# Optimization experiments

Measured on AMD Instinct MI355X. Metric: run time of the kernel, lower is better.

Reference implementation:

```python
import jax, jax.numpy as jnp
import numpy as np

E = 200000          # number of edges
MUL = 32            # multiplicity per irrep in irreps_in1/irreps_out
NT = 2              # num_tensors_in1
U = MUL * NT        # 64: combined multiplicity after fuse_in
SCALAR_DIM = 64     # irreps_edge_scalars num_irreps
HID = 64            # radial MLP hidden width
WNUM = 2 * U        # 128: LinearScaleWithWeights weight_numel (64 for 0e + 64 for 1o)
PW = 0.125          # uvw path weight sqrt(dim_out/ (u*v)) combined with 3j: all paths -> 1/8
INV_S3 = 1.0 / np.sqrt(3.0)

# e3nn normalize2mom constant for silu: 1/sqrt(E[silu(z)^2]), z ~ N(0,1)
_z = np.linspace(-12.0, 12.0, 200001)
_phi = np.exp(-0.5 * _z ** 2) / np.sqrt(2.0 * np.pi)
_s = _z / (1.0 + np.exp(-_z))
SILU_CST = float(1.0 / np.sqrt(np.trapz(_s ** 2 * _phi, _z)))


def setup_inputs() -> dict:
    key = jax.random.key(0)
    ks = jax.random.split(key, 15)
    f32 = jnp.float32
    return {
        "x1a": jax.random.normal(ks[0], (E, 128), f32),   # 32x0e + 32x1o
        "x1b": jax.random.normal(ks[1], (E, 128), f32),
        "x2": jax.random.normal(ks[2], (E, 4), f32),      # 1x0e + 1x1o
        "scalars": jax.random.normal(ks[3], (E, SCALAR_DIM), f32),
        # main tensor-product weights, one (u=64, w=32) block per instruction (v=1 squeezed)
        "w0": jax.random.normal(ks[4], (U, MUL), f32),    # 0e x 0e -> 0e (slot 0)
        "w1": jax.random.normal(ks[5], (U, MUL), f32),    # 1o x 1o -> 0e (slot 1)
        "w2": jax.random.normal(ks[6], (U, MUL), f32),    # 0e x 1o -> 1o (slot 2)
        "w3": jax.random.normal(ks[7], (U, MUL), f32),    # 1o x 0e -> 1o (slot 3)
        # LinearScaleWithWeights.linear_out: 64x0e+64x1o -> 32x0e+32x1o
        "Wl0": jax.random.normal(ks[8], (U, MUL), f32),
        "Wl1": jax.random.normal(ks[9], (U, MUL), f32),
        # radial MLP (e3nn FullyConnectedNet [64,64,64,128], silu)
        "Wm1": jax.random.normal(ks[10], (SCALAR_DIM, HID), f32),
        "Wm2": jax.random.normal(ks[11], (HID, HID), f32),
        "Wm3": jax.random.normal(ks[12], (HID, WNUM), f32),
        # final o3.Linear: 32x0e+32x1o -> 32x0e+32x1o
        "Wf0": jax.random.normal(ks[13], (MUL, MUL), f32),
        "Wf1": jax.random.normal(ks[14], (MUL, MUL), f32),
    }


def reference(x1a, x1b, x2, scalars, w0, w1, w2, w3, Wl0, Wl1, Wm1, Wm2, Wm3, Wf0, Wf1):
    n = x1a.shape[0]
    # fuse_in: stack heads then regroup per irrep -> combined 64x0e + 64x1o layout
    s0 = jnp.concatenate([x1a[:, :MUL], x1b[:, :MUL]], axis=1)                    # [E, 64]
    s1 = jnp.concatenate([x1a[:, MUL:].reshape(n, MUL, 3),
                          x1b[:, MUL:].reshape(n, MUL, 3)], axis=1)               # [E, 64, 3]
    y0 = x2[:, 0:1]    # 1x0e
    y1 = x2[:, 1:4]    # 1x1o

    # weight generator: e3nn FullyConnectedNet with normalized silu
    h = SILU_CST * jax.nn.silu((scalars @ Wm1) / jnp.sqrt(jnp.float32(SCALAR_DIM)))
    h = SILU_CST * jax.nn.silu((h @ Wm2) / jnp.sqrt(jnp.float32(HID)))
    weights = (h @ Wm3) / jnp.sqrt(jnp.float32(HID))                              # [E, 128]

    # main TensorProduct -> irreps_mid = 32x0e + 32x0e + 32x1o + 32x1o
    mid0 = PW * jnp.einsum('eu,uw->ew', s0 * y0, w0)                              # [E, 32]
    mid1 = (PW * INV_S3) * jnp.einsum('eu,uw->ew',
                                      jnp.einsum('euk,ek->eu', s1, y1), w1)       # [E, 32]
    mid2 = PW * jnp.einsum('eu,uw,ek->ewk', s0, w2, y1)                           # [E, 32, 3]
    mid3 = PW * jnp.einsum('euk,uw->ewk', s1 * y0[:, :, None], w3)                # [E, 32, 3]
    m0 = jnp.concatenate([mid0, mid1], axis=1)                                    # [E, 64] 0e
    m1 = jnp.concatenate([mid2, mid3], axis=1)                                    # [E, 64, 3] 1o

    # LinearScaleWithWeights: per-edge elementwise scale (uvu tp vs ones), then o3.Linear
    m0 = m0 * weights[:, :U]
    m1 = m1 * weights[:, U:, None]
    o0 = jnp.einsum('eu,uw->ew', m0, Wl0) / jnp.sqrt(jnp.float32(U))              # [E, 32]
    o1 = jnp.einsum('euk,uw->ewk', m1, Wl1) / jnp.sqrt(jnp.float32(U))            # [E, 32, 3]

    # final o3.Linear on irreps_out
    o0 = jnp.einsum('eu,uw->ew', o0, Wf0) / jnp.sqrt(jnp.float32(MUL))
    o1 = jnp.einsum('euk,uw->ewk', o1, Wf1) / jnp.sqrt(jnp.float32(MUL))
    return jnp.concatenate([o0, o1.reshape(n, MUL * 3)], axis=1)                  # [E, 128]
```

## Files before the change

### kernel.cpp

```cpp
#include <hip/hip_runtime.h>
#include <math.h>


#define TPB 256
#define ET  64
#define SAS 68

#define FMA4(acc, s, b)                                         \
  acc.x = fmaf((s), (b).x, acc.x); acc.y = fmaf((s), (b).y, acc.y); \
  acc.z = fmaf((s), (b).z, acc.z); acc.w = fmaf((s), (b).w, acc.w)

__global__ void zero_cst_kernel(double* cst) {
  if (threadIdx.x == 0) cst[0] = 0.0;
}

__global__ void cst_accum_kernel(double* cst) {
  __shared__ double red[256];
  double sum = 0.0;
  for (long i = (long)blockIdx.x * 256 + threadIdx.x; i <= 200000; i += 64L * 256) {
    double z = -12.0 + (double)i * (24.0 / 200000.0);
    double s = z / (1.0 + exp(-z));
    double phi = exp(-0.5 * z * z) * 0.3989422804014327;
    double f = s * s * phi;
    if (i == 0 || i == 200000) f *= 0.5;
    sum += f;
  }
  red[threadIdx.x] = sum;
  __syncthreads();
  for (int off = 128; off > 0; off >>= 1) {
    if (threadIdx.x < (unsigned)off) red[threadIdx.x] += red[threadIdx.x + off];
    __syncthreads();
  }
  if (threadIdx.x == 0) atomicAdd(cst, red[0]);
}

__global__ void prep_C_kernel(const float* __restrict__ Wl0, const float* __restrict__ Wf0,
                              const float* __restrict__ Wl1, const float* __restrict__ Wf1,
                              float* __restrict__ C0, float* __restrict__ C1) {
  const float* Wl = blockIdx.x ? Wl1 : Wl0;
  const float* Wf = blockIdx.x ? Wf1 : Wf0;
  float* C = blockIdx.x ? C1 : C0;
  for (int i = threadIdx.x; i < 64 * 32; i += 256) {
    int u = i >> 5, w = i & 31;
    float acc = 0.f;
#pragma unroll
    for (int v = 0; v < 32; ++v) acc = fmaf(Wl[u * 32 + v], Wf[v * 32 + w], acc);
    C[i] = acc * 0.022097086912079612f;
  }
}

__device__ __forceinline__ void stageB(const float* __restrict__ g, int ncols, int col0,
                                       float* __restrict__ sB, int t) {
#pragma unroll
  for (int r = 0; r < 2; ++r) {
    int i = (r * TPB + t) * 4;
    int c = i >> 5, j = i & 31;
    *(float4*)(sB + i) = *(const float4*)(g + c * ncols + col0 + j);
  }
}

__device__ __forceinline__ void gemm2(const float* __restrict__ sA,
                                      const float* __restrict__ sB,
                                      int e0l, int e1l, int cg,
                                      float4& out0, float4& out1) {
  float4 acc0 = make_float4(0.f, 0.f, 0.f, 0.f);
  float4 acc1 = make_float4(0.f, 0.f, 0.f, 0.f);
  const float* a0p = sA + e0l * SAS;
  const float* a1p = sA + e1l * SAS;
  const float* bp  = sB + 4 * cg;
#pragma unroll 4
  for (int c4 = 0; c4 < 16; ++c4) {
    float4 a0 = *(const float4*)(a0p + 4 * c4);
    float4 a1 = *(const float4*)(a1p + 4 * c4);
    const float* bb = bp + c4 * 128;
    float4 b0 = *(const float4*)(bb);
    float4 b1 = *(const float4*)(bb + 32);
    float4 b2 = *(const float4*)(bb + 64);
    float4 b3 = *(const float4*)(bb + 96);
    FMA4(acc0, a0.x, b0); FMA4(acc1, a1.x, b0);
    FMA4(acc0, a0.y, b1); FMA4(acc1, a1.y, b1);
    FMA4(acc0, a0.z, b2); FMA4(acc1, a1.z, b2);
    FMA4(acc0, a0.w, b3); FMA4(acc1, a1.w, b3);
  }
  out0 = acc0;
  out1 = acc1;
}

__device__ __forceinline__ float silu1(float x, float cst) {
  x *= 0.125f;
  return cst * x / (1.f + __expf(-x));
}

__device__ __forceinline__ float4 siluq(float4 v, float cst) {
  return make_float4(silu1(v.x, cst), silu1(v.y, cst), silu1(v.z, cst), silu1(v.w, cst));
}

__device__ __forceinline__ float4 muls(float4 a, float s) {
  return make_float4(a.x * s, a.y * s, a.z * s, a.w * s);
}

__device__ __forceinline__ float4 cmul(float4 a, float4 b, float s) {
  return make_float4(s * a.x * b.x, s * a.y * b.y, s * a.z * b.z, s * a.w * b.w);
}

__global__ __launch_bounds__(TPB, 4) void fused_tp(
    const float* __restrict__ x1a, const float* __restrict__ x1b,
    const float* __restrict__ x2, const float* __restrict__ scalars,
    const float* __restrict__ w0, const float* __restrict__ w1,
    const float* __restrict__ w2, const float* __restrict__ w3,
    const float* __restrict__ Wm1, const float* __restrict__ Wm2,
    const float* __restrict__ Wm3, const float* __restrict__ C0,
    const float* __restrict__ C1, const double* __restrict__ cstp,
    float* __restrict__ out) {
  __shared__ float sA[ET * SAS];
  __shared__ float sB0[64 * 32];
  __shared__ float sB1[64 * 32];
  __shared__ float sY[ET * 4];

  const int t  = threadIdx.x;
  const int cg = t & 7;
  const int eh = t >> 3;
  const long e0 = (long)blockIdx.x * ET;
  const float cst = (float)(1.0 / sqrt(cstp[0] * (24.0 / 200000.0)));

  const float pw   = 0.125f;
  const float pws3 = 0.125f * 0.57735026918962576f;

  if (t < ET) *(float4*)(sY + 4 * t) = *(const float4*)(x2 + (e0 + t) * 4);
#pragma unroll
  for (int r = 0; r < 4; ++r) {
    int i = r * TPB + t; int e = i >> 4; int j4 = (i & 15) << 2;
    *(float4*)(sA + e * SAS + j4) = *(const float4*)(scalars + (e0 + e) * 64 + j4);
  }
  stageB(Wm1, 64, 0, sB0, t);
  stageB(Wm1, 64, 32, sB1, t);
  __syncthreads();

  float4 h0a, h0b, h1a, h1b;
  {
    float4 r0, r1;
    gemm2(sA, sB0, eh, eh + 32, cg, r0, r1);
    h0a = siluq(r0, cst); h1a = siluq(r1, cst);
    gemm2(sA, sB1, eh, eh + 32, cg, r0, r1);
    h0b = siluq(r0, cst); h1b = siluq(r1, cst);
  }
  __syncthreads();

  *(float4*)(sA + eh * SAS + 4 * cg)        = h0a;
  *(float4*)(sA + eh * SAS + 32 + 4 * cg)   = h0b;
  *(float4*)(sA + (eh + 32) * SAS + 4 * cg)      = h1a;
  *(float4*)(sA + (eh + 32) * SAS + 32 + 4 * cg) = h1b;
  stageB(Wm2, 64, 0, sB0, t);
  stageB(Wm2, 64, 32, sB1, t);
  __syncthreads();

  {
    float4 r0, r1;
    gemm2(sA, sB0, eh, eh + 32, cg, r0, r1);
    h0a = siluq(r0, cst); h1a = siluq(r1, cst);
    gemm2(sA, sB1, eh, eh + 32, cg, r0, r1);
    h0b = siluq(r0, cst); h1b = siluq(r1, cst);
  }
  __syncthreads();

  *(float4*)(sA + eh * SAS + 4 * cg)        = h0a;
  *(float4*)(sA + eh * SAS + 32 + 4 * cg)   = h0b;
  *(float4*)(sA + (eh + 32) * SAS + 4 * cg)      = h1a;
  *(float4*)(sA + (eh + 32) * SAS + 32 + 4 * cg) = h1b;
  stageB(Wm3, 128, 0, sB0, t);
  stageB(Wm3, 128, 32, sB1, t);
  __syncthreads();

  float4 wq[2][4];
  {
    float4 r0, r1;
    gemm2(sA, sB0, eh, eh + 32, cg, r0, r1);
    wq[0][0] = muls(r0, 0.125f); wq[1][0] = muls(r1, 0.125f);
    gemm2(sA, sB1, eh, eh + 32, cg, r0, r1);
    wq[0][1] = muls(r0, 0.125f); wq[1][1] = muls(r1, 0.125f);
  }
  __syncthreads();
  stageB(Wm3, 128, 64, sB0, t);
  stageB(Wm3, 128, 96, sB1, t);
  __syncthreads();
  {
    float4 r0, r1;
    gemm2(sA, sB0, eh, eh + 32, cg, r0, r1);
    wq[0][2] = muls(r0, 0.125f); wq[1][2] = muls(r1, 0.125f);
    gemm2(sA, sB1, eh, eh + 32, cg, r0, r1);
    wq[0][3] = muls(r0, 0.125f); wq[1][3] = muls(r1, 0.125f);
  }
  __syncthreads();

#pragma unroll
  for (int r = 0; r < 4; ++r) {
    int i = r * TPB + t; int e = i >> 4; int j4 = (i & 15) << 2;
    const float* src = (j4 < 32) ? (x1a + (e0 + e) * 128 + j4)
                                 : (x1b + (e0 + e) * 128 + j4 - 32);
    *(float4*)(sA + e * SAS + j4) = *(const float4*)src;
  }
  stageB(w0, 32, 0, sB0, t);
  stageB(w2, 32, 0, sB1, t);
  __syncthreads();
  float4 m0q[2], p2q[2];
  gemm2(sA, sB0, eh, eh + 32, cg, m0q[0], m0q[1]);
  gemm2(sA, sB1, eh, eh + 32, cg, p2q[0], p2q[1]);
  __syncthreads();

#pragma unroll 2
  for (int r = 0; r < 16; ++r) {
    int i = r * TPB + t; int e = i >> 6; int u = i & 63;
    const float* xr = ((u < 32) ? x1a : x1b) + (e0 + e) * 128 + 32 + 3 * (u & 31);
    const float* yr = sY + e * 4;
    sA[e * SAS + u] = xr[0] * yr[1] + xr[1] * yr[2] + xr[2] * yr[3];
  }
  stageB(w1, 32, 0, sB0, t);
  stageB(w3, 32, 0, sB1, t);
  __syncthreads();
  float4 m1q[2];
  gemm2(sA, sB0, eh, eh + 32, cg, m1q[0], m1q[1]);
  __syncthreads();

#pragma unroll
  for (int ei = 0; ei < 2; ++ei) {
    int e = eh + 32 * ei;
    float y0v = sY[e * 4];
    *(float4*)(sA + e * SAS + 4 * cg)      = cmul(m0q[ei], wq[ei][0], pw * y0v);
    *(float4*)(sA + e * SAS + 32 + 4 * cg) = cmul(m1q[ei], wq[ei][1], pws3);
  }
  stageB(C0, 32, 0, sB0, t);
  __syncthreads();
  float4 o0q[2];
  gemm2(sA, sB0, eh, eh + 32, cg, o0q[0], o0q[1]);
  __syncthreads();

  stageB(C1, 32, 0, sB0, t);
  float o1v[2][12];
#pragma unroll
  for (int k = 0; k < 3; ++k) {
#pragma unroll 2
    for (int r = 0; r < 16; ++r) {
      int i = r * TPB + t; int e = i >> 6; int u = i & 63;
      const float* xr = ((u < 32) ? x1a : x1b) + (e0 + e) * 128 + 32 + 3 * (u & 31);
      sA[e * SAS + u] = xr[k];
    }
    __syncthreads();
    float4 t3[2];
    gemm2(sA, sB1, eh, eh + 32, cg, t3[0], t3[1]);
    __syncthreads();
#pragma unroll
    for (int ei = 0; ei < 2; ++ei) {
      int e = eh + 32 * ei;
      float y0v = sY[e * 4];
      float y1k = sY[e * 4 + 1 + k];
      *(float4*)(sA + e * SAS + 4 * cg)      = cmul(p2q[ei], wq[ei][2], pw * y1k);
      *(float4*)(sA + e * SAS + 32 + 4 * cg) = cmul(t3[ei], wq[ei][3], pw * y0v);
    }
    __syncthreads();
    float4 r0, r1;
    gemm2(sA, sB0, eh, eh + 32, cg, r0, r1);
    o1v[0][0 + k] = r0.x; o1v[0][3 + k] = r0.y; o1v[0][6 + k] = r0.z; o1v[0][9 + k] = r0.w;
    o1v[1][0 + k] = r1.x; o1v[1][3 + k] = r1.y; o1v[1][6 + k] = r1.z; o1v[1][9 + k] = r1.w;
    __syncthreads();
  }

#pragma unroll
  for (int ei = 0; ei < 2; ++ei) {
    long eg = e0 + eh + 32 * ei;
    float* ob = out + eg * 128;
    *(float4*)(ob + 4 * cg) = o0q[ei];
    float* o1b = ob + 32 + 12 * cg;
    *(float4*)(o1b)     = make_float4(o1v[ei][0], o1v[ei][1], o1v[ei][2],  o1v[ei][3]);
    *(float4*)(o1b + 4) = make_float4(o1v[ei][4], o1v[ei][5], o1v[ei][6],  o1v[ei][7]);
    *(float4*)(o1b + 8) = make_float4(o1v[ei][8], o1v[ei][9], o1v[ei][10], o1v[ei][11]);
  }
}

extern "C" void kernel_launch(void* const* d_in, const int* in_sizes, int n_in,
                              void* d_out, int out_size, void* d_ws, size_t ws_size,
                              hipStream_t stream) {
  const float* x1a     = (const float*)d_in[0];
  const float* x1b     = (const float*)d_in[1];
  const float* x2      = (const float*)d_in[2];
  const float* scalars = (const float*)d_in[3];
  const float* w0      = (const float*)d_in[4];
  const float* w1      = (const float*)d_in[5];
  const float* w2      = (const float*)d_in[6];
  const float* w3      = (const float*)d_in[7];
  const float* Wl0     = (const float*)d_in[8];
  const float* Wl1     = (const float*)d_in[9];
  const float* Wm1     = (const float*)d_in[10];
  const float* Wm2     = (const float*)d_in[11];
  const float* Wm3     = (const float*)d_in[12];
  const float* Wf0     = (const float*)d_in[13];
  const float* Wf1     = (const float*)d_in[14];
  float* out = (float*)d_out;

  double* cst = (double*)d_ws;
  float* C0 = (float*)d_ws + 128;
  float* C1 = C0 + 64 * 32;

  const int E = in_sizes[0] / 128;
  const int nblocks = E / ET;

  zero_cst_kernel<<<1, 64, 0, stream>>>(cst);
  cst_accum_kernel<<<64, 256, 0, stream>>>(cst);
  prep_C_kernel<<<2, 256, 0, stream>>>(Wl0, Wf0, Wl1, Wf1, C0, C1);
  fused_tp<<<nblocks, TPB, 0, stream>>>(x1a, x1b, x2, scalars, w0, w1, w2, w3,
                                        Wm1, Wm2, Wm3, C0, C1, cst, out);
}
```

Measured before the change: 481.4 us.

## Hoist k-independent GEMMs out of the 1o loop and merge prep kernels

```diff
diff --git a/kernel.cpp b/kernel.cpp
--- a/kernel.cpp
+++ b/kernel.cpp
@@ -3,49 +3,46 @@
 
 
 #define TPB 256
-#define ET  64
 #define SAS 68
 
 #define FMA4(acc, s, b)                                         \
   acc.x = fmaf((s), (b).x, acc.x); acc.y = fmaf((s), (b).y, acc.y); \
   acc.z = fmaf((s), (b).z, acc.z); acc.w = fmaf((s), (b).w, acc.w)
 
-__global__ void zero_cst_kernel(double* cst) {
-  if (threadIdx.x == 0) cst[0] = 0.0;
-}
-
-__global__ void cst_accum_kernel(double* cst) {
-  __shared__ double red[256];
-  double sum = 0.0;
-  for (long i = (long)blockIdx.x * 256 + threadIdx.x; i <= 200000; i += 64L * 256) {
-    double z = -12.0 + (double)i * (24.0 / 200000.0);
-    double s = z / (1.0 + exp(-z));
-    double phi = exp(-0.5 * z * z) * 0.3989422804014327;
-    double f = s * s * phi;
-    if (i == 0 || i == 200000) f *= 0.5;
-    sum += f;
-  }
-  red[threadIdx.x] = sum;
-  __syncthreads();
-  for (int off = 128; off > 0; off >>= 1) {
-    if (threadIdx.x < (unsigned)off) red[threadIdx.x] += red[threadIdx.x + off];
-    __syncthreads();
-  }
-  if (threadIdx.x == 0) atomicAdd(cst, red[0]);
-}
-
-__global__ void prep_C_kernel(const float* __restrict__ Wl0, const float* __restrict__ Wf0,
-                              const float* __restrict__ Wl1, const float* __restrict__ Wf1,
-                              float* __restrict__ C0, float* __restrict__ C1) {
-  const float* Wl = blockIdx.x ? Wl1 : Wl0;
-  const float* Wf = blockIdx.x ? Wf1 : Wf0;
-  float* C = blockIdx.x ? C1 : C0;
-  for (int i = threadIdx.x; i < 64 * 32; i += 256) {
-    int u = i >> 5, w = i & 31;
-    float acc = 0.f;
-#pragma unroll
-    for (int v = 0; v < 32; ++v) acc = fmaf(Wl[u * 32 + v], Wf[v * 32 + w], acc);
-    C[i] = acc * 0.022097086912079612f;
+__global__ void prep_kernel(const float* __restrict__ Wl0, const float* __restrict__ Wf0,
+                            const float* __restrict__ Wl1, const float* __restrict__ Wf1,
+                            float* __restrict__ C0, float* __restrict__ C1,
+                            double* __restrict__ part) {
+  if (blockIdx.x < 64) {
+    __shared__ double red[256];
+    double sum = 0.0;
+    for (long i = (long)blockIdx.x * 256 + threadIdx.x; i <= 200000; i += 64L * 256) {
+      double z = -12.0 + (double)i * (24.0 / 200000.0);
+      double s = z / (1.0 + exp(-z));
+      double phi = exp(-0.5 * z * z) * 0.3989422804014327;
+      double f = s * s * phi;
+      if (i == 0 || i == 200000) f *= 0.5;
+      sum += f;
+    }
+    red[threadIdx.x] = sum;
+    __syncthreads();
+    for (int off = 128; off > 0; off >>= 1) {
+      if (threadIdx.x < (unsigned)off) red[threadIdx.x] += red[threadIdx.x + off];
+      __syncthreads();
+    }
+    if (threadIdx.x == 0) part[blockIdx.x] = red[0];
+  } else {
+    const int b = blockIdx.x - 64;
+    const float* Wl = b ? Wl1 : Wl0;
+    const float* Wf = b ? Wf1 : Wf0;
+    float* C = b ? C1 : C0;
+    for (int i = threadIdx.x; i < 64 * 32; i += 256) {
+      int u = i >> 5, w = i & 31;
+      float acc = 0.f;
+#pragma unroll
+      for (int v = 0; v < 32; ++v) acc = fmaf(Wl[u * 32 + v], Wf[v * 32 + w], acc);
+      C[i] = acc * 0.022097086912079612f;
+    }
   }
 }
 
@@ -86,6 +83,73 @@
   out1 = acc1;
 }
 
+__device__ __forceinline__ void gemm2_dual(const float* __restrict__ sA,
+                                           const float* __restrict__ sB0,
+                                           const float* __restrict__ sB1,
+                                           int e0l, int e1l, int cg,
+                                           float4& o00, float4& o01,
+                                           float4& o10, float4& o11) {
+  float4 a00 = make_float4(0.f, 0.f, 0.f, 0.f);
+  float4 a01 = make_float4(0.f, 0.f, 0.f, 0.f);
+  float4 a10 = make_float4(0.f, 0.f, 0.f, 0.f);
+  float4 a11 = make_float4(0.f, 0.f, 0.f, 0.f);
+  const float* a0p = sA + e0l * SAS;
+  const float* a1p = sA + e1l * SAS;
+  const float* bp0 = sB0 + 4 * cg;
+  const float* bp1 = sB1 + 4 * cg;
+#pragma unroll 2
+  for (int c4 = 0; c4 < 16; ++c4) {
+    float4 a0 = *(const float4*)(a0p + 4 * c4);
+    float4 a1 = *(const float4*)(a1p + 4 * c4);
+    const float* b0b = bp0 + c4 * 128;
+    const float* b1b = bp1 + c4 * 128;
+    float4 B00 = *(const float4*)(b0b);
+    float4 B01 = *(const float4*)(b0b + 32);
+    float4 B02 = *(const float4*)(b0b + 64);
+    float4 B03 = *(const float4*)(b0b + 96);
+    float4 B10 = *(const float4*)(b1b);
+    float4 B11 = *(const float4*)(b1b + 32);
+    float4 B12 = *(const float4*)(b1b + 64);
+    float4 B13 = *(const float4*)(b1b + 96);
+    FMA4(a00, a0.x, B00); FMA4(a01, a1.x, B00);
+    FMA4(a10, a0.x, B10); FMA4(a11, a1.x, B10);
+    FMA4(a00, a0.y, B01); FMA4(a01, a1.y, B01);
+    FMA4(a10, a0.y, B11); FMA4(a11, a1.y, B11);
+    FMA4(a00, a0.z, B02); FMA4(a01, a1.z, B02);
+    FMA4(a10, a0.z, B12); FMA4(a11, a1.z, B12);
+    FMA4(a00, a0.w, B03); FMA4(a01, a1.w, B03);
+    FMA4(a10, a0.w, B13); FMA4(a11, a1.w, B13);
+  }
+  o00 = a00; o01 = a01; o10 = a10; o11 = a11;
+}
+
+__device__ __forceinline__ void gemm_k32(const float* __restrict__ sA,
+                                         const float* __restrict__ sBbase,
+                                         int e0l, int e1l, int cg,
+                                         float4& out0, float4& out1) {
+  float4 acc0 = make_float4(0.f, 0.f, 0.f, 0.f);
+  float4 acc1 = make_float4(0.f, 0.f, 0.f, 0.f);
+  const float* a0p = sA + e0l * SAS;
+  const float* a1p = sA + e1l * SAS;
+  const float* bp  = sBbase + 4 * cg;
+#pragma unroll 4
+  for (int c4 = 0; c4 < 8; ++c4) {
+    float4 a0 = *(const float4*)(a0p + 4 * c4);
+    float4 a1 = *(const float4*)(a1p + 4 * c4);
+    const float* bb = bp + c4 * 128;
+    float4 b0 = *(const float4*)(bb);
+    float4 b1 = *(const float4*)(bb + 32);
+    float4 b2 = *(const float4*)(bb + 64);
+    float4 b3 = *(const float4*)(bb + 96);
+    FMA4(acc0, a0.x, b0); FMA4(acc1, a1.x, b0);
+    FMA4(acc0, a0.y, b1); FMA4(acc1, a1.y, b1);
+    FMA4(acc0, a0.z, b2); FMA4(acc1, a1.z, b2);
+    FMA4(acc0, a0.w, b3); FMA4(acc1, a1.w, b3);
+  }
+  out0 = acc0;
+  out1 = acc1;
+}
+
 __device__ __forceinline__ float silu1(float x, float cst) {
   x *= 0.125f;
   return cst * x / (1.f + __expf(-x));
@@ -101,6 +165,10 @@
 
 __device__ __forceinline__ float4 cmul(float4 a, float4 b, float s) {
   return make_float4(s * a.x * b.x, s * a.y * b.y, s * a.z * b.z, s * a.w * b.w);
+}
+
+__device__ __forceinline__ float4 emul(float4 a, float4 b) {
+  return make_float4(a.x * b.x, a.y * b.y, a.z * b.z, a.w * b.w);
 }
 
 __global__ __launch_bounds__(TPB, 4) void fused_tp(
@@ -110,23 +178,29 @@
     const float* __restrict__ w2, const float* __restrict__ w3,
     const float* __restrict__ Wm1, const float* __restrict__ Wm2,
     const float* __restrict__ Wm3, const float* __restrict__ C0,
-    const float* __restrict__ C1, const double* __restrict__ cstp,
+    const float* __restrict__ C1, const double* __restrict__ part,
     float* __restrict__ out) {
-  __shared__ float sA[ET * SAS];
-  __shared__ float sB0[64 * 32];
-  __shared__ float sB1[64 * 32];
-  __shared__ float sY[ET * 4];
+  __shared__ __align__(16) float sA[64 * SAS];
+  __shared__ __align__(16) float sB0[64 * 32];
+  __shared__ __align__(16) float sB1[64 * 32];
+  __shared__ __align__(16) float sY[64 * 4];
+  __shared__ float scst_s;
 
   const int t  = threadIdx.x;
   const int cg = t & 7;
   const int eh = t >> 3;
-  const long e0 = (long)blockIdx.x * ET;
-  const float cst = (float)(1.0 / sqrt(cstp[0] * (24.0 / 200000.0)));
+  const long e0 = (long)blockIdx.x * 64;
 
   const float pw   = 0.125f;
   const float pws3 = 0.125f * 0.57735026918962576f;
 
-  if (t < ET) *(float4*)(sY + 4 * t) = *(const float4*)(x2 + (e0 + t) * 4);
+  if (t < 64) {
+    double v = part[t];
+#pragma unroll
+    for (int m = 32; m > 0; m >>= 1) v += __shfl_xor(v, m);
+    if (t == 0) scst_s = (float)(1.0 / sqrt(v * (24.0 / 200000.0)));
+    *(float4*)(sY + 4 * t) = *(const float4*)(x2 + (e0 + t) * 4);
+  }
 #pragma unroll
   for (int r = 0; r < 4; ++r) {
     int i = r * TPB + t; int e = i >> 4; int j4 = (i & 15) << 2;
@@ -136,60 +210,42 @@
   stageB(Wm1, 64, 32, sB1, t);
   __syncthreads();
 
-  float4 h0a, h0b, h1a, h1b;
-  {
-    float4 r0, r1;
-    gemm2(sA, sB0, eh, eh + 32, cg, r0, r1);
-    h0a = siluq(r0, cst); h1a = siluq(r1, cst);
-    gemm2(sA, sB1, eh, eh + 32, cg, r0, r1);
-    h0b = siluq(r0, cst); h1b = siluq(r1, cst);
-  }
-  __syncthreads();
-
-  *(float4*)(sA + eh * SAS + 4 * cg)        = h0a;
-  *(float4*)(sA + eh * SAS + 32 + 4 * cg)   = h0b;
-  *(float4*)(sA + (eh + 32) * SAS + 4 * cg)      = h1a;
-  *(float4*)(sA + (eh + 32) * SAS + 32 + 4 * cg) = h1b;
+  const float cst = scst_s;
+  const float4 yv0 = *(const float4*)(sY + eh * 4);
+  const float4 yv1 = *(const float4*)(sY + (eh + 32) * 4);
+
+  float4 r00, r01, r10, r11;
+  gemm2_dual(sA, sB0, sB1, eh, eh + 32, cg, r00, r01, r10, r11);
+  __syncthreads();
+  *(float4*)(sA + eh * SAS + 4 * cg)             = siluq(r00, cst);
+  *(float4*)(sA + eh * SAS + 32 + 4 * cg)        = siluq(r10, cst);
+  *(float4*)(sA + (eh + 32) * SAS + 4 * cg)      = siluq(r01, cst);
+  *(float4*)(sA + (eh + 32) * SAS + 32 + 4 * cg) = siluq(r11, cst);
   stageB(Wm2, 64, 0, sB0, t);
   stageB(Wm2, 64, 32, sB1, t);
   __syncthreads();
 
-  {
-    float4 r0, r1;
-    gemm2(sA, sB0, eh, eh + 32, cg, r0, r1);
-    h0a = siluq(r0, cst); h1a = siluq(r1, cst);
-    gemm2(sA, sB1, eh, eh + 32, cg, r0, r1);
-    h0b = siluq(r0, cst); h1b = siluq(r1, cst);
-  }
-  __syncthreads();
-
-  *(float4*)(sA + eh * SAS + 4 * cg)        = h0a;
-  *(float4*)(sA + eh * SAS + 32 + 4 * cg)   = h0b;
-  *(float4*)(sA + (eh + 32) * SAS + 4 * cg)      = h1a;
-  *(float4*)(sA + (eh + 32) * SAS + 32 + 4 * cg) = h1b;
+  gemm2_dual(sA, sB0, sB1, eh, eh + 32, cg, r00, r01, r10, r11);
+  __syncthreads();
+  *(float4*)(sA + eh * SAS + 4 * cg)             = siluq(r00, cst);
+  *(float4*)(sA + eh * SAS + 32 + 4 * cg)        = siluq(r10, cst);
+  *(float4*)(sA + (eh + 32) * SAS + 4 * cg)      = siluq(r01, cst);
+  *(float4*)(sA + (eh + 32) * SAS + 32 + 4 * cg) = siluq(r11, cst);
   stageB(Wm3, 128, 0, sB0, t);
   stageB(Wm3, 128, 32, sB1, t);
   __syncthreads();
 
-  float4 wq[2][4];
-  {
-    float4 r0, r1;
-    gemm2(sA, sB0, eh, eh + 32, cg, r0, r1);
-    wq[0][0] = muls(r0, 0.125f); wq[1][0] = muls(r1, 0.125f);
-    gemm2(sA, sB1, eh, eh + 32, cg, r0, r1);
-    wq[0][1] = muls(r0, 0.125f); wq[1][1] = muls(r1, 0.125f);
-  }
+  float4 gq0[2], gq1[2], gq2[2], gq3[2];
+  gemm2_dual(sA, sB0, sB1, eh, eh + 32, cg, r00, r01, r10, r11);
+  gq0[0] = muls(r00, 0.125f); gq0[1] = muls(r01, 0.125f);
+  gq1[0] = muls(r10, 0.125f); gq1[1] = muls(r11, 0.125f);
   __syncthreads();
   stageB(Wm3, 128, 64, sB0, t);
   stageB(Wm3, 128, 96, sB1, t);
   __syncthreads();
-  {
-    float4 r0, r1;
-    gemm2(sA, sB0, eh, eh + 32, cg, r0, r1);
-    wq[0][2] = muls(r0, 0.125f); wq[1][2] = muls(r1, 0.125f);
-    gemm2(sA, sB1, eh, eh + 32, cg, r0, r1);
-    wq[0][3] = muls(r0, 0.125f); wq[1][3] = muls(r1, 0.125f);
-  }
+  gemm2_dual(sA, sB0, sB1, eh, eh + 32, cg, r00, r01, r10, r11);
+  gq2[0] = muls(r00, 0.125f); gq2[1] = muls(r01, 0.125f);
+  gq3[0] = muls(r10, 0.125f); gq3[1] = muls(r11, 0.125f);
   __syncthreads();
 
 #pragma unroll
@@ -202,42 +258,63 @@
   stageB(w0, 32, 0, sB0, t);
   stageB(w2, 32, 0, sB1, t);
   __syncthreads();
-  float4 m0q[2], p2q[2];
-  gemm2(sA, sB0, eh, eh + 32, cg, m0q[0], m0q[1]);
-  gemm2(sA, sB1, eh, eh + 32, cg, p2q[0], p2q[1]);
-  __syncthreads();
-
-#pragma unroll 2
-  for (int r = 0; r < 16; ++r) {
-    int i = r * TPB + t; int e = i >> 6; int u = i & 63;
-    const float* xr = ((u < 32) ? x1a : x1b) + (e0 + e) * 128 + 32 + 3 * (u & 31);
+
+  float4 m0g[2], p2g[2], w3g[2];
+  gemm2_dual(sA, sB0, sB1, eh, eh + 32, cg, r00, r01, r10, r11);
+  m0g[0] = cmul(r00, gq0[0], pw * yv0.x);
+  m0g[1] = cmul(r01, gq0[1], pw * yv1.x);
+  p2g[0] = cmul(r10, gq2[0], pw);
+  p2g[1] = cmul(r11, gq2[1], pw);
+  w3g[0] = muls(gq3[0], pw * yv0.x);
+  w3g[1] = muls(gq3[1], pw * yv1.x);
+  __syncthreads();
+
+#pragma unroll
+  for (int r = 0; r < 4; ++r) {
+    int i = r * TPB + t; int e = i >> 4; int u4 = i & 15;
+    const float* src = ((u4 < 8) ? x1a : x1b) + (e0 + e) * 128 + 32 + 12 * (u4 & 7);
+    float4 va = *(const float4*)(src);
+    float4 vb = *(const float4*)(src + 4);
+    float4 vc = *(const float4*)(src + 8);
     const float* yr = sY + e * 4;
-    sA[e * SAS + u] = xr[0] * yr[1] + xr[1] * yr[2] + xr[2] * yr[3];
+    float4 tv;
+    tv.x = va.x * yr[1] + va.y * yr[2] + va.z * yr[3];
+    tv.y = va.w * yr[1] + vb.x * yr[2] + vb.y * yr[3];
+    tv.z = vb.z * yr[1] + vb.w * yr[2] + vc.x * yr[3];
+    tv.w = vc.y * yr[1] + vc.z * yr[2] + vc.w * yr[3];
+    *(float4*)(sA + e * SAS + 4 * u4) = tv;
   }
   stageB(w1, 32, 0, sB0, t);
-  stageB(w3, 32, 0, sB1, t);
-  __syncthreads();
+  stageB(C0, 32, 0, sB1, t);
+  __syncthreads();
+
   float4 m1q[2];
   gemm2(sA, sB0, eh, eh + 32, cg, m1q[0], m1q[1]);
   __syncthreads();
 
-#pragma unroll
-  for (int ei = 0; ei < 2; ++ei) {
-    int e = eh + 32 * ei;
-    float y0v = sY[e * 4];
-    *(float4*)(sA + e * SAS + 4 * cg)      = cmul(m0q[ei], wq[ei][0], pw * y0v);
-    *(float4*)(sA + e * SAS + 32 + 4 * cg) = cmul(m1q[ei], wq[ei][1], pws3);
-  }
-  stageB(C0, 32, 0, sB0, t);
-  __syncthreads();
+  *(float4*)(sA + eh * SAS + 4 * cg)             = m0g[0];
+  *(float4*)(sA + eh * SAS + 32 + 4 * cg)        = cmul(m1q[0], gq1[0], pws3);
+  *(float4*)(sA + (eh + 32) * SAS + 4 * cg)      = m0g[1];
+  *(float4*)(sA + (eh + 32) * SAS + 32 + 4 * cg) = cmul(m1q[1], gq1[1], pws3);
+  __syncthreads();
+
   float4 o0q[2];
-  gemm2(sA, sB0, eh, eh + 32, cg, o0q[0], o0q[1]);
-  __syncthreads();
-
-  stageB(C1, 32, 0, sB0, t);
+  gemm2(sA, sB1, eh, eh + 32, cg, o0q[0], o0q[1]);
+  __syncthreads();
+
+  *(float4*)(sA + eh * SAS + 4 * cg)        = p2g[0];
+  *(float4*)(sA + (eh + 32) * SAS + 4 * cg) = p2g[1];
+  stageB(w3, 32, 0, sB0, t);
+  stageB(C1, 32, 0, sB1, t);
+  __syncthreads();
+
+  float4 q2q[2];
+  gemm_k32(sA, sB1, eh, eh + 32, cg, q2q[0], q2q[1]);
+
   float o1v[2][12];
 #pragma unroll
   for (int k = 0; k < 3; ++k) {
+    __syncthreads();
 #pragma unroll 2
     for (int r = 0; r < 16; ++r) {
       int i = r * TPB + t; int e = i >> 6; int u = i & 63;
@@ -246,22 +323,23 @@
     }
     __syncthreads();
     float4 t3[2];
-    gemm2(sA, sB1, eh, eh + 32, cg, t3[0], t3[1]);
-    __syncthreads();
-#pragma unroll
-    for (int ei = 0; ei < 2; ++ei) {
-      int e = eh + 32 * ei;
-      float y0v = sY[e * 4];
-      float y1k = sY[e * 4 + 1 + k];
-      *(float4*)(sA + e * SAS + 4 * cg)      = cmul(p2q[ei], wq[ei][2], pw * y1k);
-      *(float4*)(sA + e * SAS + 32 + 4 * cg) = cmul(t3[ei], wq[ei][3], pw * y0v);
-    }
-    __syncthreads();
-    float4 r0, r1;
-    gemm2(sA, sB0, eh, eh + 32, cg, r0, r1);
-    o1v[0][0 + k] = r0.x; o1v[0][3 + k] = r0.y; o1v[0][6 + k] = r0.z; o1v[0][9 + k] = r0.w;
-    o1v[1][0 + k] = r1.x; o1v[1][3 + k] = r1.y; o1v[1][6 + k] = r1.z; o1v[1][9 + k] = r1.w;
-    __syncthreads();
+    gemm2(sA, sB0, eh, eh + 32, cg, t3[0], t3[1]);
+    __syncthreads();
+    *(float4*)(sA + eh * SAS + 4 * cg)        = emul(t3[0], w3g[0]);
+    *(float4*)(sA + (eh + 32) * SAS + 4 * cg) = emul(t3[1], w3g[1]);
+    __syncthreads();
+    float4 q3a, q3b;
+    gemm_k32(sA, sB1 + 1024, eh, eh + 32, cg, q3a, q3b);
+    float ya = (k == 0) ? yv0.y : (k == 1) ? yv0.z : yv0.w;
+    float yb = (k == 0) ? yv1.y : (k == 1) ? yv1.z : yv1.w;
+    o1v[0][0 + k] = ya * q2q[0].x + q3a.x;
+    o1v[0][3 + k] = ya * q2q[0].y + q3a.y;
+    o1v[0][6 + k] = ya * q2q[0].z + q3a.z;
+    o1v[0][9 + k] = ya * q2q[0].w + q3a.w;
+    o1v[1][0 + k] = yb * q2q[1].x + q3b.x;
+    o1v[1][3 + k] = yb * q2q[1].y + q3b.y;
+    o1v[1][6 + k] = yb * q2q[1].z + q3b.z;
+    o1v[1][9 + k] = yb * q2q[1].w + q3b.w;
   }
 
 #pragma unroll
@@ -296,16 +374,14 @@
   const float* Wf1     = (const float*)d_in[14];
   float* out = (float*)d_out;
 
-  double* cst = (double*)d_ws;
+  double* part = (double*)d_ws;
   float* C0 = (float*)d_ws + 128;
   float* C1 = C0 + 64 * 32;
 
   const int E = in_sizes[0] / 128;
-  const int nblocks = E / ET;
-
-  zero_cst_kernel<<<1, 64, 0, stream>>>(cst);
-  cst_accum_kernel<<<64, 256, 0, stream>>>(cst);
-  prep_C_kernel<<<2, 256, 0, stream>>>(Wl0, Wf0, Wl1, Wf1, C0, C1);
+  const int nblocks = E / 64;
+
+  prep_kernel<<<66, 256, 0, stream>>>(Wl0, Wf0, Wl1, Wf1, C0, C1, part);
   fused_tp<<<nblocks, TPB, 0, stream>>>(x1a, x1b, x2, scalars, w0, w1, w2, w3,
-                                        Wm1, Wm2, Wm3, C0, C1, cst, out);
-}
+                                        Wm1, Wm2, Wm3, C0, C1, part, out);
+}
```

Measured after the change: 450.3 us. 1.07x faster.
